# Kernel tuning notes

Hardware: AMD Instinct MI355X
Metric: run time of the kernel (lower is better)

Reference implementation:

```python
import jax, jax.numpy as jnp
import numpy as np

N_NODES = 100000
N_EDGES = 3200000
FEAT = 256
HID = 128
OUT = 64
HOPS = 3


def setup_inputs() -> dict:
    key = jax.random.key(0)
    ks = jax.random.split(key, 10)
    return {
        "feature_source": jax.random.normal(ks[0], (N_NODES, FEAT), jnp.float32),
        "feature_target": jax.random.normal(ks[1], (N_NODES, FEAT), jnp.float32),
        "edge_row": jax.random.randint(ks[2], (N_EDGES,), 0, N_NODES, jnp.int32),
        "edge_col": jax.random.randint(ks[3], (N_EDGES,), 0, N_NODES, jnp.int32),
        "edge_w": jax.random.uniform(ks[4], (N_EDGES,), jnp.float32),
        "W_src": jax.random.normal(ks[5], (FEAT, HID), jnp.float32) * 0.02,
        "b_src": jnp.zeros((HID,), jnp.float32),
        "W_tgt": jax.random.normal(ks[6], (FEAT, HID), jnp.float32) * 0.02,
        "b_tgt": jnp.zeros((HID,), jnp.float32),
        "w_s": jnp.ones((HOPS + 1, 1), jnp.float32),
        "w_t": jnp.ones((HOPS + 1, 1), jnp.float32),
        "W_node": jax.random.normal(ks[7], (2 * HID, OUT), jnp.float32) * 0.02,
        "b_node": jnp.zeros((OUT,), jnp.float32),
    }


def _spmm(row, col, w, x):
    # (sparse adj)[row, col] = w ; out[i] = sum_{e: row[e]=i} w[e] * x[col[e]]
    return jax.ops.segment_sum(w[:, None] * x[col], row, num_segments=N_NODES)


def reference(feature_source, feature_target, edge_row, edge_col, edge_w,
              W_src, b_src, W_tgt, b_tgt, w_s, w_t, W_node, b_node):
    x_s = feature_source @ W_src + b_src  # [N, HID]
    x_t = feature_target @ W_tgt + b_tgt  # [N, HID]
    feat_s = w_s[0] * x_s
    feat_t = w_t[0] * x_t
    curr_s, curr_t = x_s, x_t
    for h in range(1, HOPS + 1):
        curr_s = _spmm(edge_row, edge_col, edge_w, curr_s)          # adj   @ curr_s
        curr_t = _spmm(edge_col, edge_row, edge_w, curr_t)          # adj_t @ curr_t
        feat_s = feat_s + w_s[h] * curr_s
        feat_t = feat_t + w_t[h] * curr_t
    feat = jnp.concatenate([feat_s, feat_t], axis=1)  # [N, 2*HID]
    # dropout is identity in eval mode; query_edges is None -> node path
    return feat @ W_node + b_node
```

## Files before the change

kernel.cpp:

```cpp
#include <hip/hip_runtime.h>

#define N_NODES 100000
#define N_EDGES 3200000
#define FEAT 256
#define HID 128
#define OUT 64
#define HOPS 3

#define NPAD 100352
#define NTOT (2 * NPAD)
#define NBUCK 196
#define CAP 36864
#define RPS 1028
#define EPB 2048

typedef unsigned short ushort_t;

__device__ __forceinline__ float bf2f(ushort_t u) {
    return __uint_as_float(((unsigned)u) << 16);
}
__device__ __forceinline__ float bflo(unsigned u) { return __uint_as_float(u << 16); }
__device__ __forceinline__ float bfhi(unsigned u) { return __uint_as_float(u & 0xffff0000u); }
__device__ __forceinline__ unsigned pack_bf16(float a, float b) {
    unsigned ua = __float_as_uint(a);
    unsigned ub = __float_as_uint(b);
    ua += 0x7fffu + ((ua >> 16) & 1u);
    ub += 0x7fffu + ((ub >> 16) & 1u);
    return (ua >> 16) | (ub & 0xffff0000u);
}

__global__ __launch_bounds__(64) void wcomb_k(
    const float* __restrict__ Wsrc, const float* __restrict__ Wtgt,
    const float* __restrict__ bsrc, const float* __restrict__ btgt,
    const float* __restrict__ Wn,
    float* __restrict__ Wc,
    float* __restrict__ bc)
{
    const int blk = blockIdx.x;
    const int j = threadIdx.x;
    if (blk < 512) {
        const float* Wsel = (blk < 256) ? Wsrc : Wtgt;
        const int i = blk & 255;
        const int koff = (blk < 256) ? 0 : HID;
        float acc = 0.f;
        for (int k = 0; k < HID; ++k)
            acc = fmaf(Wsel[i * HID + k], Wn[(koff + k) * OUT + j], acc);
        Wc[blk * OUT + j] = acc;
    } else {
        const float* bsel = (blk == 512) ? bsrc : btgt;
        const int koff = (blk == 512) ? 0 : HID;
        float acc = 0.f;
        for (int k = 0; k < HID; ++k)
            acc = fmaf(bsel[k], Wn[(koff + k) * OUT + j], acc);
        bc[(blk - 512) * OUT + j] = acc;
    }
}

__global__ __launch_bounds__(256) void gemm_in(
    const float* __restrict__ X,
    const float* __restrict__ B,
    const float* __restrict__ bias,
    ushort_t* __restrict__ h0)
{
    __shared__ __align__(16) float at[64][76];
    __shared__ __align__(16) float bs[64][OUT];
    const int tid = threadIdx.x;
    const int tx = tid & 15;
    const int ty = tid >> 4;
    const int row0 = blockIdx.x * 64;

    float acc[4][4];
#pragma unroll
    for (int r = 0; r < 4; ++r)
#pragma unroll
        for (int c = 0; c < 4; ++c) acc[r][c] = 0.f;

    for (int chunk = 0; chunk < 4; ++chunk) {
        const int kbase = chunk * 64;
        {
            int lc = tid & 15, lr = tid >> 4;
#pragma unroll
            for (int p = 0; p < 4; ++p) {
                int r = lr + p * 16;
                int grow = row0 + r; if (grow > N_NODES - 1) grow = N_NODES - 1;
                float4 v = *(const float4*)(X + (size_t)grow * FEAT + kbase + lc * 4);
                float vv[4] = {v.x, v.y, v.z, v.w};
#pragma unroll
                for (int i = 0; i < 4; ++i) {
                    int ii = (i + lc) & 3;
                    at[lc * 4 + ii][r] = vv[ii];
                }
            }
        }
        {
            int jf = tid & 15, kk0 = tid >> 4;
#pragma unroll
            for (int p = 0; p < 4; ++p) {
                int kk = kk0 + p * 16;
                *(float4*)&bs[kk][jf * 4] =
                    *(const float4*)(B + (size_t)(kbase + kk) * OUT + jf * 4);
            }
        }
        __syncthreads();
#pragma unroll 8
        for (int kk = 0; kk < 64; ++kk) {
            float4 a = *(const float4*)&at[kk][ty * 4];
            float4 b = *(const float4*)&bs[kk][tx * 4];
            float av[4] = {a.x, a.y, a.z, a.w};
            float bv[4] = {b.x, b.y, b.z, b.w};
#pragma unroll
            for (int r = 0; r < 4; ++r)
#pragma unroll
                for (int c = 0; c < 4; ++c)
                    acc[r][c] = fmaf(av[r], bv[c], acc[r][c]);
        }
        __syncthreads();
    }

    float4 bj = *(const float4*)(bias + tx * 4);
    float bjv[4] = {bj.x, bj.y, bj.z, bj.w};
#pragma unroll
    for (int r = 0; r < 4; ++r) {
        int grow = row0 + ty * 4 + r;
        if (grow < N_NODES) {
            float o[4];
#pragma unroll
            for (int c = 0; c < 4; ++c) o[c] = acc[r][c] + bjv[c];
            size_t off = (size_t)grow * OUT + tx * 4;
            *(uint2*)(h0 + off) = make_uint2(pack_bf16(o[0], o[1]), pack_bf16(o[2], o[3]));
        }
    }
}

__global__ __launch_bounds__(256) void init_k(int* __restrict__ bcur) {
    int t = threadIdx.x;
    if (t < NBUCK) bcur[t] = t * CAP;
}

__global__ __launch_bounds__(256) void fill_p1(
    const int* __restrict__ erow, const int* __restrict__ ecol,
    const float* __restrict__ ew,
    int* __restrict__ bcur, int2* __restrict__ meta_tmp)
{
    __shared__ int2 stage[2 * EPB];
    __shared__ unsigned char bkt[2 * EPB];
    __shared__ int lcnt[256], loff[256], gbase[256], cur[256];
    __shared__ int sdata[256];
    const int tid = threadIdx.x;
    const int base = blockIdx.x * EPB;
    const int n = min(EPB, N_EDGES - base);

    int r[8], c[8], wb[8];
    lcnt[tid] = 0;
    __syncthreads();
#pragma unroll
    for (int k = 0; k < 8; ++k) {
        int i = k * 256 + tid;
        if (i < n) {
            int e = base + i;
            r[k] = erow[e];
            c[k] = ecol[e];
            wb[k] = __float_as_int(ew[e]);
            atomicAdd(&lcnt[r[k] >> 10], 1);
            atomicAdd(&lcnt[(NPAD + c[k]) >> 10], 1);
        } else {
            r[k] = -1;
        }
    }
    __syncthreads();
    sdata[tid] = lcnt[tid];
    __syncthreads();
    for (int off = 1; off < 256; off <<= 1) {
        int t = (tid >= off) ? sdata[tid - off] : 0;
        __syncthreads();
        sdata[tid] += t;
        __syncthreads();
    }
    loff[tid] = sdata[tid] - lcnt[tid];
    cur[tid] = loff[tid];
    gbase[tid] = (lcnt[tid] > 0) ? atomicAdd(&bcur[tid], lcnt[tid]) : 0;
    __syncthreads();
#pragma unroll
    for (int k = 0; k < 8; ++k) {
        if (r[k] >= 0) {
            int bs_ = r[k] >> 10;
            int l = atomicAdd(&cur[bs_], 1);
            stage[l] = make_int2(c[k] | ((r[k] & 1023) << 17), wb[k]);
            bkt[l] = (unsigned char)bs_;
            int ut = NPAD + c[k];
            int bt_ = ut >> 10;
            int l2 = atomicAdd(&cur[bt_], 1);
            stage[l2] = make_int2(r[k] | ((ut & 1023) << 17), wb[k]);
            bkt[l2] = (unsigned char)bt_;
        }
    }
    __syncthreads();
    const int tot = 2 * n;
    for (int i = tid; i < tot; i += 256) {
        int b = bkt[i];
        meta_tmp[(size_t)gbase[b] + (i - loff[b])] = stage[i];
    }
}

__global__ __launch_bounds__(256) void fill_p2(
    const int* __restrict__ bcur,
    const int2* __restrict__ meta_tmp,
    int2* __restrict__ meta, int* __restrict__ rowptr)
{
    __shared__ int cnt[1024];
    __shared__ int sdata[256];
    const int tid = threadIdx.x;
    const int b = blockIdx.x;
    const int seg0 = b * CAP;
    const int seg1 = bcur[b];

    for (int i = tid; i < 1024; i += 256) cnt[i] = 0;
    __syncthreads();
    for (int j = seg0 + tid; j < seg1; j += 256) {
        int2 e = meta_tmp[j];
        atomicAdd(&cnt[(e.x >> 17) & 1023], 1);
    }
    __syncthreads();
    int4 v = *(int4*)&cnt[tid * 4];
    int tsum = v.x + v.y + v.z + v.w;
    sdata[tid] = tsum;
    __syncthreads();
    for (int off = 1; off < 256; off <<= 1) {
        int t = (tid >= off) ? sdata[tid - off] : 0;
        __syncthreads();
        sdata[tid] += t;
        __syncthreads();
    }
    int excl = sdata[tid] - tsum;
    int4 o;
    o.x = seg0 + excl;
    o.y = o.x + v.x;
    o.z = o.y + v.y;
    o.w = o.z + v.z;
    *(int4*)(rowptr + b * RPS + tid * 4) = o;
    *(int4*)&cnt[tid * 4] = o;
    if (tid == 0) rowptr[b * RPS + 1024] = seg1;
    __syncthreads();
    for (int j = seg0 + tid; j < seg1; j += 256) {
        int2 e = meta_tmp[j];
        int pos = atomicAdd(&cnt[(e.x >> 17) & 1023], 1);
        meta[pos] = make_int2((e.x & 0x1ffff) << 7, e.y);
    }
}

__global__ __launch_bounds__(256) void spmm_k(
    const int* __restrict__ rowptr,
    const int2* __restrict__ meta,
    const ushort_t* __restrict__ xs, const ushort_t* __restrict__ xt,
    ushort_t* __restrict__ ns, ushort_t* __restrict__ nt)
{
    const int unit = blockIdx.x * 4 + (threadIdx.x >> 6);
    const int lane = threadIdx.x & 63;
    const int q  = lane >> 4;
    const int sl = lane & 15;

    const ushort_t* x; ushort_t* nxt;
    int node;
    if (unit < NPAD) {
        node = unit;
        if (node >= N_NODES) return;
        x = xs; nxt = ns;
    } else {
        node = unit - NPAD;
        if (node >= N_NODES) return;
        x = xt; nxt = nt;
    }

    const int rbase = (unit >> 10) * RPS + (unit & 1023);
    const int start = rowptr[rbase];
    const int end   = rowptr[rbase + 1];

    float a0 = 0.f, a1 = 0.f, a2 = 0.f, a3 = 0.f;
    const int coffb = sl * 8;
    const char* xb = (const char*)x;

    int jb = start;
    int2 m0, m1, m2, m3;
    bool have = (jb + 15 < end);
    if (have) {
        m0 = meta[jb + q];
        m1 = meta[jb + 4 + q];
        m2 = meta[jb + 8 + q];
        m3 = meta[jb + 12 + q];
    }
    while (have) {
        uint2 u0 = *(const uint2*)(xb + (unsigned)m0.x + coffb);
        uint2 u1 = *(const uint2*)(xb + (unsigned)m1.x + coffb);
        uint2 u2 = *(const uint2*)(xb + (unsigned)m2.x + coffb);
        uint2 u3 = *(const uint2*)(xb + (unsigned)m3.x + coffb);
        float w0 = __int_as_float(m0.y), w1 = __int_as_float(m1.y);
        float w2 = __int_as_float(m2.y), w3 = __int_as_float(m3.y);

        const int jn = jb + 16;
        have = (jn + 15 < end);
        if (have) {
            m0 = meta[jn + q];
            m1 = meta[jn + 4 + q];
            m2 = meta[jn + 8 + q];
            m3 = meta[jn + 12 + q];
        }
        jb = jn;

        a0 = fmaf(w0, bflo(u0.x), a0);
        a1 = fmaf(w0, bfhi(u0.x), a1);
        a2 = fmaf(w0, bflo(u0.y), a2);
        a3 = fmaf(w0, bfhi(u0.y), a3);
        a0 = fmaf(w1, bflo(u1.x), a0);
        a1 = fmaf(w1, bfhi(u1.x), a1);
        a2 = fmaf(w1, bflo(u1.y), a2);
        a3 = fmaf(w1, bfhi(u1.y), a3);
        a0 = fmaf(w2, bflo(u2.x), a0);
        a1 = fmaf(w2, bfhi(u2.x), a1);
        a2 = fmaf(w2, bflo(u2.y), a2);
        a3 = fmaf(w2, bfhi(u2.y), a3);
        a0 = fmaf(w3, bflo(u3.x), a0);
        a1 = fmaf(w3, bfhi(u3.x), a1);
        a2 = fmaf(w3, bflo(u3.y), a2);
        a3 = fmaf(w3, bfhi(u3.y), a3);
    }

    if (jb < end) {
        int jj0 = jb + q,      jj1 = jb + 4 + q;
        int jj2 = jb + 8 + q,  jj3 = jb + 12 + q;
        bool v0 = jj0 < end, v1 = jj1 < end, v2 = jj2 < end, v3 = jj3 < end;
        int2 t0 = meta[v0 ? jj0 : start];
        int2 t1 = meta[v1 ? jj1 : start];
        int2 t2 = meta[v2 ? jj2 : start];
        int2 t3 = meta[v3 ? jj3 : start];
        uint2 u0 = *(const uint2*)(xb + (unsigned)t0.x + coffb);
        uint2 u1 = *(const uint2*)(xb + (unsigned)t1.x + coffb);
        uint2 u2 = *(const uint2*)(xb + (unsigned)t2.x + coffb);
        uint2 u3 = *(const uint2*)(xb + (unsigned)t3.x + coffb);
        float w0 = v0 ? __int_as_float(t0.y) : 0.f;
        float w1 = v1 ? __int_as_float(t1.y) : 0.f;
        float w2 = v2 ? __int_as_float(t2.y) : 0.f;
        float w3 = v3 ? __int_as_float(t3.y) : 0.f;
        a0 = fmaf(w0, bflo(u0.x), a0);
        a1 = fmaf(w0, bfhi(u0.x), a1);
        a2 = fmaf(w0, bflo(u0.y), a2);
        a3 = fmaf(w0, bfhi(u0.y), a3);
        a0 = fmaf(w1, bflo(u1.x), a0);
        a1 = fmaf(w1, bfhi(u1.x), a1);
        a2 = fmaf(w1, bflo(u1.y), a2);
        a3 = fmaf(w1, bfhi(u1.y), a3);
        a0 = fmaf(w2, bflo(u2.x), a0);
        a1 = fmaf(w2, bfhi(u2.x), a1);
        a2 = fmaf(w2, bflo(u2.y), a2);
        a3 = fmaf(w2, bfhi(u2.y), a3);
        a0 = fmaf(w3, bflo(u3.x), a0);
        a1 = fmaf(w3, bfhi(u3.x), a1);
        a2 = fmaf(w3, bflo(u3.y), a2);
        a3 = fmaf(w3, bfhi(u3.y), a3);
    }

    a0 += __shfl_xor(a0, 16, 64);
    a1 += __shfl_xor(a1, 16, 64);
    a2 += __shfl_xor(a2, 16, 64);
    a3 += __shfl_xor(a3, 16, 64);
    a0 += __shfl_xor(a0, 32, 64);
    a1 += __shfl_xor(a1, 32, 64);
    a2 += __shfl_xor(a2, 32, 64);
    a3 += __shfl_xor(a3, 32, 64);

    if (q == 0) {
        *(uint2*)(nxt + ((size_t)node << 6) + sl * 4) =
            make_uint2(pack_bf16(a0, a1), pack_bf16(a2, a3));
    }
}

__global__ __launch_bounds__(256) void combine_k(
    const ushort_t* __restrict__ s0, const ushort_t* __restrict__ s1,
    const ushort_t* __restrict__ s2, const ushort_t* __restrict__ s3,
    const ushort_t* __restrict__ t0, const ushort_t* __restrict__ t1,
    const ushort_t* __restrict__ t2, const ushort_t* __restrict__ t3,
    const float* __restrict__ wsv, const float* __restrict__ wtv,
    const float* __restrict__ bn,
    float* __restrict__ out)
{
    const int gid = blockIdx.x * 256 + threadIdx.x;
    if (gid >= N_NODES * (OUT / 4)) return;
    const size_t off = (size_t)gid * 4;

    float4 b = ((const float4*)bn)[gid & (OUT / 4 - 1)];
    float acc[4] = {b.x, b.y, b.z, b.w};

    const ushort_t* bufs[8] = {s0, s1, s2, s3, t0, t1, t2, t3};
    float w[8];
#pragma unroll
    for (int h = 0; h < 4; ++h) { w[h] = wsv[h]; w[4 + h] = wtv[h]; }

#pragma unroll
    for (int h = 0; h < 8; ++h) {
        ushort4 u = *(const ushort4*)(bufs[h] + off);
        acc[0] = fmaf(w[h], bf2f(u.x), acc[0]);
        acc[1] = fmaf(w[h], bf2f(u.y), acc[1]);
        acc[2] = fmaf(w[h], bf2f(u.z), acc[2]);
        acc[3] = fmaf(w[h], bf2f(u.w), acc[3]);
    }
    *(float4*)(out + off) = make_float4(acc[0], acc[1], acc[2], acc[3]);
}

extern "C" void kernel_launch(void* const* d_in, const int* in_sizes, int n_in,
                              void* d_out, int out_size, void* d_ws, size_t ws_size,
                              hipStream_t stream) {
    const float* fsrc = (const float*)d_in[0];
    const float* ftgt = (const float*)d_in[1];
    const int*   erow = (const int*)d_in[2];
    const int*   ecol = (const int*)d_in[3];
    const float* ew   = (const float*)d_in[4];
    const float* Wsrc = (const float*)d_in[5];
    const float* bsrc = (const float*)d_in[6];
    const float* Wtgt = (const float*)d_in[7];
    const float* btgt = (const float*)d_in[8];
    const float* ws   = (const float*)d_in[9];
    const float* wt   = (const float*)d_in[10];
    const float* Wn   = (const float*)d_in[11];
    const float* bn   = (const float*)d_in[12];
    float* out = (float*)d_out;

    const size_t buf = (size_t)N_NODES * OUT;
    char* p = (char*)d_ws;
    ushort_t* hs[4]; ushort_t* ht[4];
    for (int h = 0; h < 4; ++h) {
        hs[h] = (ushort_t*)p; p += buf * 2;
        ht[h] = (ushort_t*)p; p += buf * 2;
    }
    int2* meta     = (int2*)p;  p += (size_t)NBUCK * CAP * 8;
    int2* meta_tmp = (int2*)p;  p += (size_t)NBUCK * CAP * 8;
    int* rowptr    = (int*)p;   p += (size_t)NBUCK * RPS * 4 + 64;
    float* Wc      = (float*)p; p += 512 * OUT * 4;
    float* bc      = (float*)p; p += 128 * 4;
    int* bcur      = (int*)p;   p += 256 * 4;

    const int eblocks = (N_EDGES + EPB - 1) / EPB;
    const int gblocks = (N_NODES + 63) / 64;

    wcomb_k<<<514, 64, 0, stream>>>(Wsrc, Wtgt, bsrc, btgt, Wn, Wc, bc);

    gemm_in<<<gblocks, 256, 0, stream>>>(fsrc, Wc, bc, hs[0]);
    gemm_in<<<gblocks, 256, 0, stream>>>(ftgt, Wc + 256 * OUT, bc + OUT, ht[0]);

    init_k<<<1, 256, 0, stream>>>(bcur);
    fill_p1<<<eblocks, 256, 0, stream>>>(erow, ecol, ew, bcur, meta_tmp);
    fill_p2<<<NBUCK, 256, 0, stream>>>(bcur, meta_tmp, meta, rowptr);

    const int sblocks = NTOT / 4;
    for (int h = 1; h <= HOPS; ++h) {
        spmm_k<<<sblocks, 256, 0, stream>>>(rowptr, meta,
                                            hs[h - 1], ht[h - 1], hs[h], ht[h]);
    }

    combine_k<<<(N_NODES * (OUT / 4) + 255) / 256, 256, 0, stream>>>(
        hs[0], hs[1], hs[2], hs[3], ht[0], ht[1], ht[2], ht[3], ws, wt, bn, out);
}
```

Before: 705.0 us.

## Fuse final SpMM hop with combine and sort edges by column sub-bucket

The third SpMM hop now also does the weighted hop combination and bias add, writing the float output directly. This removes the separate combine kernel and the write and re-read of the last-hop bf16 buffers. fill_p2 also splits each row's edges into 4 sub-bins by column bits, so the gathers within a row are loosely sorted by column, which may improve cache locality. The fused kernel runs half as many waves, each doing two row gathers in sequence, which may reduce latency hiding.

```diff
diff --git a/kernel.cpp b/kernel.cpp
--- a/kernel.cpp
+++ b/kernel.cpp
@@ -207,22 +207,25 @@
     const int2* __restrict__ meta_tmp,
     int2* __restrict__ meta, int* __restrict__ rowptr)
 {
-    __shared__ int cnt[1024];
+    __shared__ int cnt[4096];
     __shared__ int sdata[256];
     const int tid = threadIdx.x;
     const int b = blockIdx.x;
     const int seg0 = b * CAP;
     const int seg1 = bcur[b];
 
-    for (int i = tid; i < 1024; i += 256) cnt[i] = 0;
+    for (int i = tid; i < 4096; i += 256) cnt[i] = 0;
     __syncthreads();
     for (int j = seg0 + tid; j < seg1; j += 256) {
         int2 e = meta_tmp[j];
-        atomicAdd(&cnt[(e.x >> 17) & 1023], 1);
-    }
-    __syncthreads();
-    int4 v = *(int4*)&cnt[tid * 4];
-    int tsum = v.x + v.y + v.z + v.w;
+        int bin = (((e.x >> 17) & 1023) << 2) | ((e.x >> 15) & 3);
+        atomicAdd(&cnt[bin], 1);
+    }
+    __syncthreads();
+    int vals[16];
+    int tsum = 0;
+#pragma unroll
+    for (int k = 0; k < 16; ++k) { vals[k] = cnt[tid * 16 + k]; tsum += vals[k]; }
     sdata[tid] = tsum;
     __syncthreads();
     for (int off = 1; off < 256; off <<= 1) {
@@ -231,53 +234,36 @@
         sdata[tid] += t;
         __syncthreads();
     }
-    int excl = sdata[tid] - tsum;
-    int4 o;
-    o.x = seg0 + excl;
-    o.y = o.x + v.x;
-    o.z = o.y + v.y;
-    o.w = o.z + v.z;
-    *(int4*)(rowptr + b * RPS + tid * 4) = o;
-    *(int4*)&cnt[tid * 4] = o;
+    int run = seg0 + sdata[tid] - tsum;
+    int rp[4];
+#pragma unroll
+    for (int k = 0; k < 16; ++k) {
+        if ((k & 3) == 0) rp[k >> 2] = run;
+        int c = vals[k];
+        cnt[tid * 16 + k] = run;
+        run += c;
+    }
+    *(int4*)(rowptr + b * RPS + tid * 4) = make_int4(rp[0], rp[1], rp[2], rp[3]);
     if (tid == 0) rowptr[b * RPS + 1024] = seg1;
     __syncthreads();
     for (int j = seg0 + tid; j < seg1; j += 256) {
         int2 e = meta_tmp[j];
-        int pos = atomicAdd(&cnt[(e.x >> 17) & 1023], 1);
+        int bin = (((e.x >> 17) & 1023) << 2) | ((e.x >> 15) & 3);
+        int pos = atomicAdd(&cnt[bin], 1);
         meta[pos] = make_int2((e.x & 0x1ffff) << 7, e.y);
     }
 }
 
-__global__ __launch_bounds__(256) void spmm_k(
-    const int* __restrict__ rowptr,
-    const int2* __restrict__ meta,
-    const ushort_t* __restrict__ xs, const ushort_t* __restrict__ xt,
-    ushort_t* __restrict__ ns, ushort_t* __restrict__ nt)
-{
-    const int unit = blockIdx.x * 4 + (threadIdx.x >> 6);
-    const int lane = threadIdx.x & 63;
-    const int q  = lane >> 4;
-    const int sl = lane & 15;
-
-    const ushort_t* x; ushort_t* nxt;
-    int node;
-    if (unit < NPAD) {
-        node = unit;
-        if (node >= N_NODES) return;
-        x = xs; nxt = ns;
-    } else {
-        node = unit - NPAD;
-        if (node >= N_NODES) return;
-        x = xt; nxt = nt;
-    }
-
+__device__ __forceinline__ void row_gather(
+    const int* __restrict__ rowptr, const int2* __restrict__ meta,
+    const char* __restrict__ xb, int unit, int q, int coffb,
+    float& a0, float& a1, float& a2, float& a3)
+{
     const int rbase = (unit >> 10) * RPS + (unit & 1023);
     const int start = rowptr[rbase];
     const int end   = rowptr[rbase + 1];
 
-    float a0 = 0.f, a1 = 0.f, a2 = 0.f, a3 = 0.f;
-    const int coffb = sl * 8;
-    const char* xb = (const char*)x;
+    a0 = 0.f; a1 = 0.f; a2 = 0.f; a3 = 0.f;
 
     int jb = start;
     int2 m0, m1, m2, m3;
@@ -357,6 +343,33 @@
         a2 = fmaf(w3, bflo(u3.y), a2);
         a3 = fmaf(w3, bfhi(u3.y), a3);
     }
+}
+
+__global__ __launch_bounds__(256) void spmm_k(
+    const int* __restrict__ rowptr,
+    const int2* __restrict__ meta,
+    const ushort_t* __restrict__ xs, const ushort_t* __restrict__ xt,
+    ushort_t* __restrict__ ns, ushort_t* __restrict__ nt)
+{
+    const int unit = blockIdx.x * 4 + (threadIdx.x >> 6);
+    const int lane = threadIdx.x & 63;
+    const int q  = lane >> 4;
+    const int sl = lane & 15;
+
+    const ushort_t* x; ushort_t* nxt;
+    int node;
+    if (unit < NPAD) {
+        node = unit;
+        if (node >= N_NODES) return;
+        x = xs; nxt = ns;
+    } else {
+        node = unit - NPAD;
+        if (node >= N_NODES) return;
+        x = xt; nxt = nt;
+    }
+
+    float a0, a1, a2, a3;
+    row_gather(rowptr, meta, (const char*)x, unit, q, sl * 8, a0, a1, a2, a3);
 
     a0 += __shfl_xor(a0, 16, 64);
     a1 += __shfl_xor(a1, 16, 64);
@@ -373,36 +386,63 @@
     }
 }
 
-__global__ __launch_bounds__(256) void combine_k(
+__global__ __launch_bounds__(256) void spmm_last(
+    const int* __restrict__ rowptr,
+    const int2* __restrict__ meta,
+    const ushort_t* __restrict__ xs, const ushort_t* __restrict__ xt,
     const ushort_t* __restrict__ s0, const ushort_t* __restrict__ s1,
-    const ushort_t* __restrict__ s2, const ushort_t* __restrict__ s3,
     const ushort_t* __restrict__ t0, const ushort_t* __restrict__ t1,
-    const ushort_t* __restrict__ t2, const ushort_t* __restrict__ t3,
     const float* __restrict__ wsv, const float* __restrict__ wtv,
     const float* __restrict__ bn,
     float* __restrict__ out)
 {
-    const int gid = blockIdx.x * 256 + threadIdx.x;
-    if (gid >= N_NODES * (OUT / 4)) return;
-    const size_t off = (size_t)gid * 4;
-
-    float4 b = ((const float4*)bn)[gid & (OUT / 4 - 1)];
-    float acc[4] = {b.x, b.y, b.z, b.w};
-
-    const ushort_t* bufs[8] = {s0, s1, s2, s3, t0, t1, t2, t3};
-    float w[8];
-#pragma unroll
-    for (int h = 0; h < 4; ++h) { w[h] = wsv[h]; w[4 + h] = wtv[h]; }
-
-#pragma unroll
-    for (int h = 0; h < 8; ++h) {
-        ushort4 u = *(const ushort4*)(bufs[h] + off);
-        acc[0] = fmaf(w[h], bf2f(u.x), acc[0]);
-        acc[1] = fmaf(w[h], bf2f(u.y), acc[1]);
-        acc[2] = fmaf(w[h], bf2f(u.z), acc[2]);
-        acc[3] = fmaf(w[h], bf2f(u.w), acc[3]);
-    }
-    *(float4*)(out + off) = make_float4(acc[0], acc[1], acc[2], acc[3]);
+    const int node = blockIdx.x * 4 + (threadIdx.x >> 6);
+    const int lane = threadIdx.x & 63;
+    const int q  = lane >> 4;
+    const int sl = lane & 15;
+    if (node >= N_NODES) return;
+    const int coffb = sl * 8;
+
+    float a0, a1, a2, a3, b0, b1, b2, b3;
+    row_gather(rowptr, meta, (const char*)xs, node, q, coffb, a0, a1, a2, a3);
+    row_gather(rowptr, meta, (const char*)xt, NPAD + node, q, coffb, b0, b1, b2, b3);
+
+    a0 += __shfl_xor(a0, 16, 64);  b0 += __shfl_xor(b0, 16, 64);
+    a1 += __shfl_xor(a1, 16, 64);  b1 += __shfl_xor(b1, 16, 64);
+    a2 += __shfl_xor(a2, 16, 64);  b2 += __shfl_xor(b2, 16, 64);
+    a3 += __shfl_xor(a3, 16, 64);  b3 += __shfl_xor(b3, 16, 64);
+    a0 += __shfl_xor(a0, 32, 64);  b0 += __shfl_xor(b0, 32, 64);
+    a1 += __shfl_xor(a1, 32, 64);  b1 += __shfl_xor(b1, 32, 64);
+    a2 += __shfl_xor(a2, 32, 64);  b2 += __shfl_xor(b2, 32, 64);
+    a3 += __shfl_xor(a3, 32, 64);  b3 += __shfl_xor(b3, 32, 64);
+
+    if (q == 0) {
+        const size_t ho = ((size_t)node << 6) + sl * 4;
+        uint2 us0 = *(const uint2*)(s0 + ho);
+        uint2 us1 = *(const uint2*)(s1 + ho);
+        uint2 us2 = *(const uint2*)(xs + ho);
+        uint2 ut0 = *(const uint2*)(t0 + ho);
+        uint2 ut1 = *(const uint2*)(t1 + ho);
+        uint2 ut2 = *(const uint2*)(xt + ho);
+        float ws0 = wsv[0], ws1 = wsv[1], ws2 = wsv[2], ws3 = wsv[3];
+        float wt0 = wtv[0], wt1 = wtv[1], wt2 = wtv[2], wt3 = wtv[3];
+        float4 bb = *(const float4*)(bn + sl * 4);
+
+        float o0 = bb.x + ws0 * bflo(us0.x) + ws1 * bflo(us1.x) + ws2 * bflo(us2.x)
+                 + ws3 * a0 + wt0 * bflo(ut0.x) + wt1 * bflo(ut1.x) + wt2 * bflo(ut2.x)
+                 + wt3 * b0;
+        float o1 = bb.y + ws0 * bfhi(us0.x) + ws1 * bfhi(us1.x) + ws2 * bfhi(us2.x)
+                 + ws3 * a1 + wt0 * bfhi(ut0.x) + wt1 * bfhi(ut1.x) + wt2 * bfhi(ut2.x)
+                 + wt3 * b1;
+        float o2 = bb.z + ws0 * bflo(us0.y) + ws1 * bflo(us1.y) + ws2 * bflo(us2.y)
+                 + ws3 * a2 + wt0 * bflo(ut0.y) + wt1 * bflo(ut1.y) + wt2 * bflo(ut2.y)
+                 + wt3 * b2;
+        float o3 = bb.w + ws0 * bfhi(us0.y) + ws1 * bfhi(us1.y) + ws2 * bfhi(us2.y)
+                 + ws3 * a3 + wt0 * bfhi(ut0.y) + wt1 * bfhi(ut1.y) + wt2 * bfhi(ut2.y)
+                 + wt3 * b3;
+
+        *(float4*)(out + (size_t)node * OUT + sl * 4) = make_float4(o0, o1, o2, o3);
+    }
 }
 
 extern "C" void kernel_launch(void* const* d_in, const int* in_sizes, int n_in,
@@ -425,8 +465,8 @@
 
     const size_t buf = (size_t)N_NODES * OUT;
     char* p = (char*)d_ws;
-    ushort_t* hs[4]; ushort_t* ht[4];
-    for (int h = 0; h < 4; ++h) {
+    ushort_t* hs[3]; ushort_t* ht[3];
+    for (int h = 0; h < 3; ++h) {
         hs[h] = (ushort_t*)p; p += buf * 2;
         ht[h] = (ushort_t*)p; p += buf * 2;
     }
@@ -449,12 +489,12 @@
     fill_p1<<<eblocks, 256, 0, stream>>>(erow, ecol, ew, bcur, meta_tmp);
     fill_p2<<<NBUCK, 256, 0, stream>>>(bcur, meta_tmp, meta, rowptr);
 
-    const int sblocks = NTOT / 4;
-    for (int h = 1; h <= HOPS; ++h) {
-        spmm_k<<<sblocks, 256, 0, stream>>>(rowptr, meta,
-                                            hs[h - 1], ht[h - 1], hs[h], ht[h]);
-    }
-
-    combine_k<<<(N_NODES * (OUT / 4) + 255) / 256, 256, 0, stream>>>(
-        hs[0], hs[1], hs[2], hs[3], ht[0], ht[1], ht[2], ht[3], ws, wt, bn, out);
-}
+    spmm_k<<<NTOT / 4, 256, 0, stream>>>(rowptr, meta,
+                                         hs[0], ht[0], hs[1], ht[1]);
+    spmm_k<<<NTOT / 4, 256, 0, stream>>>(rowptr, meta,
+                                         hs[1], ht[1], hs[2], ht[2]);
+
+    spmm_last<<<NPAD / 4, 256, 0, stream>>>(rowptr, meta,
+                                            hs[2], ht[2], hs[0], hs[1],
+                                            ht[0], ht[1], ws, wt, bn, out);
+}
```

New measurement: 714.8 us. About the same (+1.4%).
